# Optimization experiments

Hardware: AMD Instinct MI355X
Metric: run time of the kernel (lower is better)

## Reference

```python
import jax, jax.numpy as jnp
import numpy as np

B, N, H, HEADS, NBINS = 64, 256, 512, 8, 3
DK = H // HEADS
NEG = -1e12

def setup_inputs() -> dict:
    key = jax.random.key(0)
    ks = jax.random.split(key, 20)
    def lin(k, out_d, in_d):
        w = jax.random.normal(k, (out_d, in_d), jnp.float32) * (1.0 / np.sqrt(in_d))
        b = jnp.zeros((out_d,), jnp.float32)
        return w, b
    x = jax.random.normal(ks[0], (B, N, H), jnp.float32)
    dist = jax.random.uniform(ks[1], (B, N - 1, N - 1), jnp.float32, 0.0, 10.0)
    dist_bar = jnp.sort(jax.random.uniform(ks[2], (B, NBINS), jnp.float32, 1.0, 9.0), axis=-1)
    mask = jnp.ones((B, N, N), jnp.float32)
    Wq, bq = lin(ks[3], H, H)
    Wk, bk = lin(ks[4], H, H)
    Wv, bv = lin(ks[5], H, H)
    Wa = jnp.stack([lin(ks[6 + i], H, H)[0] for i in range(NBINS)])  # [NBINS,H,H]
    ba = jnp.zeros((NBINS, H), jnp.float32)
    Ws1, bs1 = lin(ks[10], H, NBINS * H)
    Ws2, bs2 = lin(ks[11], H, H)
    gamma = jnp.ones((H,), jnp.float32)
    beta = jnp.zeros((H,), jnp.float32)
    return dict(x=x, dist=dist, dist_bar=dist_bar, mask=mask, Wq=Wq, bq=bq, Wk=Wk, bk=bk,
                Wv=Wv, bv=bv, Wa=Wa, ba=ba, Ws1=Ws1, bs1=bs1, Ws2=Ws2, bs2=bs2,
                gamma=gamma, beta=beta)

def reference(x, dist, dist_bar, mask, Wq, bq, Wk, bk, Wv, bv, Wa, ba, Ws1, bs1, Ws2, bs2, gamma, beta):
    residual = x
    def proj(x, W, b):  # torch Linear: x @ W.T + b
        return jnp.einsum('bnd,od->bno', x, W) + b
    def heads(t):  # [B,N,H] -> [B,heads,N,dk]
        return t.reshape(B, N, HEADS, DK).transpose(0, 2, 1, 3)
    q, k, v = heads(proj(x, Wq, bq)), heads(proj(x, Wk, bk)), heads(proj(x, Wv, bv))
    scores = jnp.einsum('bhnd,bhmd->bhnm', q, k) / jnp.sqrt(jnp.float32(DK))  # [B,heads,N,N]
    # padding mask (shape [B,1,N,N] != scores shape -> masked_fill(mask==0))
    scores = jnp.where(mask[:, None] == 0, NEG, scores)
    # new_dist: super node row/col = 1, interior = dist
    new_dist = jnp.ones((B, 1, N, N), jnp.float32).at[:, :, 1:, 1:].set(dist[:, None])
    multi_out, attn_list = [], []
    for i in range(NBINS):
        cut = dist_bar[:, i][:, None, None, None]          # per-batch threshold
        dm = new_dist < cut                                 # [B,1,N,N]
        dm = dm.at[:, :, 0, :].set(True).at[:, :, :, 0].set(True)
        sd = jnp.where(dm, scores, NEG)
        attn = jax.nn.softmax(sd, axis=-1)                  # dropout: eval mode
        attn_list.append(attn)
        multi_out.append(jnp.einsum('bhnm,bhmd->bhnd', attn, v))
    x_cat = jnp.concatenate([
        jnp.einsum('bnd,od->bno', multi_out[i].transpose(0, 2, 1, 3).reshape(B, N, H), Wa[i]) + ba[i]
        for i in range(NBINS)], axis=-1)                    # [B,N,NBINS*H]
    h = jax.nn.silu(jnp.einsum('bnd,od->bno', x_cat, Ws1) + bs1)
    h = jnp.einsum('bnd,od->bno', h, Ws2) + bs2
    h = h + residual
    mu = jnp.mean(h, axis=-1, keepdims=True)
    var = jnp.var(h, axis=-1, keepdims=True)
    out = (h - mu) / jnp.sqrt(var + 1e-6) * gamma + beta
    return (out, jnp.stack(attn_list))
```

## Files before the change

kernel.cpp:

```cpp
#include <hip/hip_runtime.h>
#include <cstddef>

#define NEGV (-1e12f)


typedef __attribute__((ext_vector_type(4))) float f32x4;
typedef __attribute__((ext_vector_type(8))) __bf16 bf16x8;

__device__ __forceinline__ unsigned short f2bf(float f) {
  union { float f; unsigned u; } v; v.f = f;
  unsigned r = v.u + 0x7FFFu + ((v.u >> 16) & 1u);
  return (unsigned short)(r >> 16);
}

#define GLDS16(gp, lp)                                                      \
  __builtin_amdgcn_global_load_lds(                                         \
      (const __attribute__((address_space(1))) void*)(gp),                  \
      (__attribute__((address_space(3))) void*)(lp), 16, 0, 0)

__global__ __launch_bounds__(256) void msa_prep(
    const float* __restrict__ x, const float* __restrict__ Wq,
    const float* __restrict__ Wk, const float* __restrict__ Wv,
    const float* __restrict__ Ws2, const float* __restrict__ Ws1,
    const float* __restrict__ Wa, const float* __restrict__ bq,
    const float* __restrict__ bk, const float* __restrict__ bv,
    const float* __restrict__ ba, const float* __restrict__ bs1,
    const float* __restrict__ dist, const float* __restrict__ dist_bar,
    const float* __restrict__ maskg,
    unsigned short* __restrict__ xb, unsigned short* __restrict__ Wqkvb,
    unsigned short* __restrict__ Ws2b, unsigned short* __restrict__ Wcatb,
    float* __restrict__ bcomb, float* __restrict__ bqkv,
    unsigned long long* __restrict__ bits) {
  __shared__ float As[16][68];
  __shared__ float Bs[16][68];
  const int blk = blockIdx.x;
  const int tid = threadIdx.x;
  if (blk < 8192) {
    int i = blk * 256 + tid;
    float4 v = ((const float4*)x)[i];
    ushort4 o; o.x = f2bf(v.x); o.y = f2bf(v.y); o.z = f2bf(v.z); o.w = f2bf(v.w);
    ((ushort4*)xb)[i] = o;
    return;
  }
  if (blk < 8960) {
    int sel = (blk - 8192) >> 8;
    int i = ((blk - 8192) & 255) * 256 + tid;
    const float* src = (sel == 0) ? Wq : (sel == 1) ? Wk : Wv;
    unsigned short* dst = Wqkvb + (size_t)sel * 262144;
    float4 v = ((const float4*)src)[i];
    ushort4 o; o.x = f2bf(v.x); o.y = f2bf(v.y); o.z = f2bf(v.z); o.w = f2bf(v.w);
    ((ushort4*)dst)[i] = o;
    return;
  }
  if (blk < 9216) {
    int i = (blk - 8960) * 256 + tid;
    float4 v = ((const float4*)Ws2)[i];
    ushort4 o; o.x = f2bf(v.x); o.y = f2bf(v.y); o.z = f2bf(v.z); o.w = f2bf(v.w);
    ((ushort4*)Ws2b)[i] = o;
    return;
  }
  if (blk < 9408) {
    const int t = blk - 9216;
    const int i = t >> 6;
    const int ob = ((t >> 3) & 7) * 64, cb = (t & 7) * 64;
    const int tx = tid & 15, ty = tid >> 4;
    float acc[4][4] = {};
    for (int kt = 0; kt < 512; kt += 16) {
      __syncthreads();
      {
        int o = tid & 63, e4 = (tid >> 6) * 4;
        float4 a4 = *(const float4*)&Ws1[(size_t)(ob + o) * 1536 + i * 512 + kt + e4];
        As[e4 + 0][o] = a4.x; As[e4 + 1][o] = a4.y;
        As[e4 + 2][o] = a4.z; As[e4 + 3][o] = a4.w;
      }
      {
        int e = tid & 15, c4 = (tid >> 4) * 4;
        float4 b4 = *(const float4*)&Wa[((size_t)i << 18) + (size_t)(kt + e) * 512 + cb + c4];
        *(float4*)&Bs[e][c4] = b4;
      }
      __syncthreads();
#pragma unroll
      for (int k = 0; k < 16; ++k) {
        float a[4], bb[4];
        *(float4*)a = *(const float4*)&As[k][ty * 4];
        *(float4*)bb = *(const float4*)&Bs[k][tx * 4];
#pragma unroll
        for (int r = 0; r < 4; ++r)
#pragma unroll
          for (int c = 0; c < 4; ++c) acc[r][c] += a[r] * bb[c];
      }
    }
#pragma unroll
    for (int r = 0; r < 4; ++r)
#pragma unroll
      for (int c = 0; c < 4; ++c)
        Wcatb[(size_t)(ob + ty * 4 + r) * 1536 + i * 512 + cb + tx * 4 + c] =
            f2bf(acc[r][c]);
    return;
  }
  if (blk < 9410) {
    int o = (blk - 9408) * 256 + tid;
    float acc = bs1[o];
    for (int cidx = 0; cidx < 1536; ++cidx)
      acc += Ws1[(size_t)o * 1536 + cidx] * ba[cidx];
    bcomb[o] = acc;
    return;
  }
  if (blk < 9411) {
    for (int i = tid; i < 1536; i += 256)
      bqkv[i] = (i < 512) ? bq[i] : (i < 1024) ? bk[i - 512] : bv[i - 1024];
    return;
  }
  {
    const int gw = (blk - 9411) * 4 + (tid >> 6);
    const int lane = tid & 63;
    const int b = gw >> 8, row = gw & 255;
    const float cut0 = dist_bar[b * 3 + 0];
    const float cut1 = dist_bar[b * 3 + 1];
    const float cut2 = dist_bar[b * 3 + 2];
    const float* mrow = maskg + (size_t)b * 65536 + (size_t)row * 256;
    const int rj = (row == 0) ? 1 : row;
    const float* drow = dist + (size_t)b * 65025 + (size_t)(rj - 1) * 255;
    unsigned long long* out = bits + (size_t)gw * 12;
#pragma unroll
    for (int cc = 0; cc < 4; ++cc) {
      const int col = cc * 64 + lane;
      const int cj = (col == 0) ? 1 : col;
      float dv = drow[cj - 1];
      bool sup = (row == 0) || (col == 0);
      bool mk = (mrow[col] != 0.f);
      if (sup) dv = -1e30f;
      unsigned long long b0 = __ballot(mk && (dv < cut0));
      unsigned long long b1 = __ballot(mk && (dv < cut1));
      unsigned long long b2 = __ballot(mk && (dv < cut2));
      if (lane == 0) { out[cc] = b0; out[4 + cc] = b1; out[8 + cc] = b2; }
    }
  }
}

template <int ACT, int RES, int OBF, int BK>
__global__ __launch_bounds__(256) void msa_gemm_mfma(
    const unsigned short* __restrict__ A, int lda,
    const unsigned short* __restrict__ W, int ldw,
    const float* __restrict__ bias, const float* __restrict__ resid,
    void* __restrict__ Cout, int ldc, int Kdim) {
  constexpr int KSUB = BK / 32;
  constexpr int RPC = BK / 8;
  constexpr int CPT = (128 * RPC) / 256;
  __shared__ __align__(16) unsigned short Asm_[2][128 * BK];
  __shared__ __align__(16) unsigned short Bsm_[2][128 * BK];
  const int tid = threadIdx.x;
  const int lane = tid & 63, wv = tid >> 6;
  const int m0 = blockIdx.x * 128, n0 = blockIdx.y * 128;
  const int wr = wv >> 1, wc = wv & 1;
  const int fr = lane & 15, fq = lane >> 4;
  f32x4 acc[4][4] = {};
  const unsigned short* Ag[CPT];
  const unsigned short* Wg[CPT];
#pragma unroll
  for (int i = 0; i < CPT; ++i) {
    int c = tid + i * 256;
    int row = c / RPC, j = c % RPC;
    Ag[i] = A + (size_t)(m0 + row) * lda + j * 8;
    Wg[i] = W + (size_t)(n0 + row) * ldw + j * 8;
  }
#pragma unroll
  for (int i = 0; i < CPT; ++i) {
    GLDS16(Ag[i], &Asm_[0][(tid + i * 256) * 8]);
    GLDS16(Wg[i], &Bsm_[0][(tid + i * 256) * 8]);
  }
  __syncthreads();
  int cur = 0;
  for (int kt = 0; kt < Kdim; kt += BK) {
    if (kt + BK < Kdim) {
      const int nx = cur ^ 1, k2 = kt + BK;
#pragma unroll
      for (int i = 0; i < CPT; ++i) {
        GLDS16(Ag[i] + k2, &Asm_[nx][(tid + i * 256) * 8]);
        GLDS16(Wg[i] + k2, &Bsm_[nx][(tid + i * 256) * 8]);
      }
    }
#pragma unroll
    for (int ks = 0; ks < KSUB; ++ks) {
      bf16x8 af[4], bfr[4];
#pragma unroll
      for (int mf = 0; mf < 4; ++mf)
        af[mf] = *(const bf16x8*)&Asm_[cur][(wr * 64 + mf * 16 + fr) * BK + ks * 32 + fq * 8];
#pragma unroll
      for (int nf = 0; nf < 4; ++nf)
        bfr[nf] = *(const bf16x8*)&Bsm_[cur][(wc * 64 + nf * 16 + fr) * BK + ks * 32 + fq * 8];
#pragma unroll
      for (int mf = 0; mf < 4; ++mf)
#pragma unroll
        for (int nf = 0; nf < 4; ++nf)
          acc[mf][nf] = __builtin_amdgcn_mfma_f32_16x16x32_bf16(
              af[mf], bfr[nf], acc[mf][nf], 0, 0, 0);
    }
    __syncthreads();
    cur ^= 1;
  }
#pragma unroll
  for (int mf = 0; mf < 4; ++mf) {
#pragma unroll
    for (int nf = 0; nf < 4; ++nf) {
      const int n = n0 + wc * 64 + nf * 16 + fr;
      const float bval = bias[n];
#pragma unroll
      for (int r = 0; r < 4; ++r) {
        const int m = m0 + wr * 64 + mf * 16 + fq * 4 + r;
        float val = acc[mf][nf][r] + bval;
        if (ACT == 1) val = val / (1.f + __expf(-val));
        if (RES == 1) val += resid[(size_t)m * ldc + n];
        if (OBF == 1)
          ((unsigned short*)Cout)[(size_t)m * ldc + n] = f2bf(val);
        else
          ((float*)Cout)[(size_t)m * ldc + n] = val;
      }
    }
  }
}

__global__ __launch_bounds__(512) void msa_fused(
    const unsigned short* __restrict__ qkvb,
    const unsigned long long* __restrict__ bits,
    float* __restrict__ attn_out, unsigned short* __restrict__ mob) {
  const int blk = blockIdx.x;
  const int b = (blk & 7) * 8 + (blk >> 6);
  const int h = (blk >> 3) & 7;
  __shared__ __align__(16) unsigned short Kl[256][72];
  __shared__ __align__(16) unsigned short Vt[64][264];
  __shared__ __align__(16) unsigned short Pl[8][16][264];
  const int tid = threadIdx.x;
  const int wv = tid >> 6, lane = tid & 63;
  const int l15 = lane & 15, fq = lane >> 4;
  {
    const unsigned short* kgp = qkvb + (size_t)(b * 256) * 1536 + 512 + h * 64;
#pragma unroll
    for (int i = 0; i < 4; ++i) {
      int s = tid + i * 512;
      int row = s >> 3, c8 = (s & 7) << 3;
      *(uint4*)&Kl[row][c8] = *(const uint4*)&kgp[(size_t)row * 1536 + c8];
    }
  }
  {
    int rv = tid & 255, half = tid >> 8;
    const unsigned short* vgp =
        qkvb + (size_t)(b * 256 + rv) * 1536 + 1024 + h * 64 + half * 32;
#pragma unroll
    for (int j4 = 0; j4 < 4; ++j4) {
      unsigned short tmp[8];
      *(uint4*)tmp = *(const uint4*)&vgp[j4 * 8];
#pragma unroll
      for (int j = 0; j < 8; ++j) Vt[half * 32 + j4 * 8 + j][rv] = tmp[j];
    }
  }
  __syncthreads();
#pragma unroll
  for (int mf = 0; mf < 2; ++mf) {
    const int r0 = wv * 32 + mf * 16;
    const unsigned short* qgp =
        qkvb + (size_t)(b * 256 + r0 + l15) * 1536 + h * 64 + fq * 8;
    bf16x8 aq0 = *(const bf16x8*)qgp;
    bf16x8 aq1 = *(const bf16x8*)(qgp + 32);
    f32x4 accs[16];
#pragma unroll
    for (int nt = 0; nt < 16; ++nt) {
      bf16x8 bk0 = *(const bf16x8*)&Kl[nt * 16 + l15][fq * 8];
      bf16x8 bk1 = *(const bf16x8*)&Kl[nt * 16 + l15][32 + fq * 8];
      f32x4 a = {};
      a = __builtin_amdgcn_mfma_f32_16x16x32_bf16(aq0, bk0, a, 0, 0, 0);
      a = __builtin_amdgcn_mfma_f32_16x16x32_bf16(aq1, bk1, a, 0, 0, 0);
      accs[nt] = a;
    }
#pragma unroll
    for (int bin = 0; bin < 3; ++bin) {
      float* pbase = attn_out + ((size_t)((bin * 64 + b) * 8 + h)) * 65536;
#pragma unroll
      for (int r = 0; r < 4; ++r) {
        const int row = r0 + fq * 4 + r;
        const unsigned long long* bw =
            bits + (size_t)(b * 256 + row) * 12 + bin * 4;
        const unsigned long long w0 = bw[0], w1 = bw[1], w2 = bw[2], w3 = bw[3];
        float p[16];
        float m = -3e38f;
#pragma unroll
        for (int nt = 0; nt < 16; ++nt) {
          unsigned long long w = (nt < 4) ? w0 : (nt < 8) ? w1 : (nt < 12) ? w2 : w3;
          unsigned keep = (unsigned)(w >> ((nt & 3) * 16 + l15)) & 1u;
          float sv = accs[nt][r] * 0.125f;
          p[nt] = keep ? sv : NEGV;
          m = fmaxf(m, p[nt]);
        }
        m = fmaxf(m, __shfl_xor(m, 1));
        m = fmaxf(m, __shfl_xor(m, 2));
        m = fmaxf(m, __shfl_xor(m, 4));
        m = fmaxf(m, __shfl_xor(m, 8));
        float sum = 0.f;
#pragma unroll
        for (int nt = 0; nt < 16; ++nt) { p[nt] = __expf(p[nt] - m); sum += p[nt]; }
        sum += __shfl_xor(sum, 1);
        sum += __shfl_xor(sum, 2);
        sum += __shfl_xor(sum, 4);
        sum += __shfl_xor(sum, 8);
        const float inv = 1.f / sum;
        float* prow = pbase + (size_t)row * 256 + l15;
#pragma unroll
        for (int nt = 0; nt < 16; ++nt) {
          float val = p[nt] * inv;
          prow[nt * 16] = val;
          Pl[wv][fq * 4 + r][nt * 16 + l15] = f2bf(val);
        }
      }
      asm volatile("s_waitcnt lgkmcnt(0)" ::: "memory");
      f32x4 acco[4] = {};
#pragma unroll
      for (int c = 0; c < 8; ++c) {
        bf16x8 pa = *(const bf16x8*)&Pl[wv][l15][c * 32 + fq * 8];
#pragma unroll
        for (int nf = 0; nf < 4; ++nf) {
          bf16x8 bv = *(const bf16x8*)&Vt[nf * 16 + l15][c * 32 + fq * 8];
          acco[nf] = __builtin_amdgcn_mfma_f32_16x16x32_bf16(pa, bv, acco[nf], 0, 0, 0);
        }
      }
#pragma unroll
      for (int nf = 0; nf < 4; ++nf)
#pragma unroll
        for (int r = 0; r < 4; ++r)
          mob[((size_t)(b * 256 + r0 + fq * 4 + r) * 3 + bin) * 512 +
              h * 64 + nf * 16 + l15] = f2bf(acco[nf][r]);
    }
  }
}

__global__ __launch_bounds__(256) void msa_mlp2ln(
    const unsigned short* __restrict__ h1b, const unsigned short* __restrict__ Ws2b,
    const float* __restrict__ bs2, const float* __restrict__ x,
    const float* __restrict__ gamma, const float* __restrict__ beta,
    float* __restrict__ outp) {
  __shared__ __align__(16) unsigned short Al[32 * 32];
  __shared__ __align__(16) unsigned short Bl[512 * 32];
  __shared__ float red[2][2][32];
  const int tid = threadIdx.x;
  const int lane = tid & 63, wv = tid >> 6;
  const int wr = wv >> 1, wc = wv & 1;
  const int l15 = lane & 15, fq = lane >> 4;
  const int m0 = blockIdx.x * 32;
  f32x4 acc[16] = {};
  for (int kt = 0; kt < 512; kt += 32) {
    if (tid < 128) {
      int row = tid >> 2, c8 = (tid & 3) * 8;
      GLDS16(h1b + (size_t)(m0 + row) * 512 + kt + c8, &Al[tid * 8]);
    }
#pragma unroll
    for (int i = 0; i < 8; ++i) {
      int c = tid + i * 256;
      int row = c >> 2, c8 = (c & 3) * 8;
      GLDS16(Ws2b + (size_t)row * 512 + kt + c8, &Bl[c * 8]);
    }
    __syncthreads();
    bf16x8 af = *(const bf16x8*)&Al[(wr * 16 + l15) * 32 + fq * 8];
#pragma unroll
    for (int nt = 0; nt < 16; ++nt) {
      bf16x8 bfr = *(const bf16x8*)&Bl[(wc * 256 + nt * 16 + l15) * 32 + fq * 8];
      acc[nt] = __builtin_amdgcn_mfma_f32_16x16x32_bf16(af, bfr, acc[nt], 0, 0, 0);
    }
    __syncthreads();
  }
  float vals[16][4];
#pragma unroll
  for (int nt = 0; nt < 16; ++nt) {
    const int n = wc * 256 + nt * 16 + l15;
    const float bval = bs2[n];
#pragma unroll
    for (int r = 0; r < 4; ++r) {
      const int m = m0 + wr * 16 + fq * 4 + r;
      vals[nt][r] = acc[nt][r] + bval + x[(size_t)m * 512 + n];
    }
  }
  const int ridx = wr * 16 + fq * 4;
#pragma unroll
  for (int r = 0; r < 4; ++r) {
    float s = 0.f;
#pragma unroll
    for (int nt = 0; nt < 16; ++nt) s += vals[nt][r];
    s += __shfl_xor(s, 1); s += __shfl_xor(s, 2);
    s += __shfl_xor(s, 4); s += __shfl_xor(s, 8);
    if (l15 == 0) red[0][wc][ridx + r] = s;
  }
  __syncthreads();
  float mu[4];
#pragma unroll
  for (int r = 0; r < 4; ++r)
    mu[r] = (red[0][0][ridx + r] + red[0][1][ridx + r]) * (1.f / 512.f);
#pragma unroll
  for (int r = 0; r < 4; ++r) {
    float s = 0.f;
#pragma unroll
    for (int nt = 0; nt < 16; ++nt) {
      float d = vals[nt][r] - mu[r];
      s += d * d;
    }
    s += __shfl_xor(s, 1); s += __shfl_xor(s, 2);
    s += __shfl_xor(s, 4); s += __shfl_xor(s, 8);
    if (l15 == 0) red[1][wc][ridx + r] = s;
  }
  __syncthreads();
  float iv[4];
#pragma unroll
  for (int r = 0; r < 4; ++r) {
    float var = (red[1][0][ridx + r] + red[1][1][ridx + r]) * (1.f / 512.f);
    iv[r] = 1.f / sqrtf(var + 1e-6f);
  }
#pragma unroll
  for (int nt = 0; nt < 16; ++nt) {
    const int n = wc * 256 + nt * 16 + l15;
    const float g = gamma[n], be = beta[n];
#pragma unroll
    for (int r = 0; r < 4; ++r) {
      const int m = m0 + wr * 16 + fq * 4 + r;
      outp[(size_t)m * 512 + n] = (vals[nt][r] - mu[r]) * iv[r] * g + be;
    }
  }
}

extern "C" void kernel_launch(void* const* d_in, const int* in_sizes, int n_in,
                              void* d_out, int out_size, void* d_ws, size_t ws_size,
                              hipStream_t stream) {
  (void)in_sizes; (void)n_in; (void)out_size; (void)ws_size;
  const float* x        = (const float*)d_in[0];
  const float* dist     = (const float*)d_in[1];
  const float* dist_bar = (const float*)d_in[2];
  const float* mask     = (const float*)d_in[3];
  const float* Wq  = (const float*)d_in[4];  const float* bq  = (const float*)d_in[5];
  const float* Wk  = (const float*)d_in[6];  const float* bk  = (const float*)d_in[7];
  const float* Wv  = (const float*)d_in[8];  const float* bv  = (const float*)d_in[9];
  const float* Wa  = (const float*)d_in[10]; const float* ba  = (const float*)d_in[11];
  const float* Ws1 = (const float*)d_in[12]; const float* bs1 = (const float*)d_in[13];
  const float* Ws2 = (const float*)d_in[14]; const float* bs2 = (const float*)d_in[15];
  const float* gamma = (const float*)d_in[16]; const float* beta = (const float*)d_in[17];

  char* w8 = (char*)d_ws;
  const size_t SZ = 8388608;
  unsigned short* qkvb = (unsigned short*)(w8 + 0);
  unsigned short* mob  = (unsigned short*)(w8 + 50331648);
  unsigned short* xb   = (unsigned short*)(w8 + 100663296);
  unsigned short* Wqkvb= (unsigned short*)(w8 + 117440512);
  unsigned short* Ws2b = (unsigned short*)(w8 + 119013376);
  unsigned short* Wcatb= (unsigned short*)(w8 + 119537664);
  float* bcomb = (float*)(w8 + 121110528);
  float* bqkv  = (float*)(w8 + 121112576);
  unsigned long long* bits = (unsigned long long*)(w8 + 121118720);
  unsigned short* h1b = qkvb;
  float* outp = (float*)d_out;
  float* attn = outp + SZ;

  msa_prep<<<13507, 256, 0, stream>>>(x, Wq, Wk, Wv, Ws2, Ws1, Wa, bq, bk, bv,
                                      ba, bs1, dist, dist_bar, mask,
                                      xb, Wqkvb, Ws2b, Wcatb, bcomb, bqkv, bits);

  msa_gemm_mfma<0, 0, 1, 32><<<dim3(128, 12), 256, 0, stream>>>(
      xb, 512, Wqkvb, 512, bqkv, nullptr, qkvb, 1536, 512);

  msa_fused<<<512, 512, 0, stream>>>(qkvb, bits, attn, mob);

  msa_gemm_mfma<1, 0, 1, 64><<<dim3(128, 4), 256, 0, stream>>>(
      mob, 1536, Wcatb, 1536, bcomb, nullptr, h1b, 512, 1536);

  msa_mlp2ln<<<512, 256, 0, stream>>>(h1b, Ws2b, bs2, x, gamma, beta, outp);
}
```

Before: 323.0 us.

## Transpose QK^T MFMA so each lane owns a query row, vectorize prob stores

Swaps the MFMA operands for the score product so each lane holds four consecutive key columns of one query row. Softmax then reduces across only two cross-lane shuffles per bin instead of four per row, and the attention probabilities are written to global memory as float4 vectors. The bf16 probabilities go to a compact, XOR-swizzled LDS tile to avoid bank conflicts, and extra waitcnt/sched barriers are added to keep LDS reuse across bins correct. The cost is higher register pressure from holding 64 probability values per lane.

```diff
diff --git a/kernel.cpp b/kernel.cpp
--- a/kernel.cpp
+++ b/kernel.cpp
@@ -229,7 +229,7 @@
   const int h = (blk >> 3) & 7;
   __shared__ __align__(16) unsigned short Kl[256][72];
   __shared__ __align__(16) unsigned short Vt[64][264];
-  __shared__ __align__(16) unsigned short Pl[8][16][264];
+  __shared__ __align__(16) unsigned short Pl[8][16][256];
   const int tid = threadIdx.x;
   const int wv = tid >> 6, lane = tid & 63;
   const int l15 = lane & 15, fq = lane >> 4;
@@ -255,11 +255,14 @@
     }
   }
   __syncthreads();
+  char* plbase = (char*)&Pl[wv][0][0];
+  const int swz = ((l15 & 1) << 6) | ((l15 & 2) << 4);
 #pragma unroll
   for (int mf = 0; mf < 2; ++mf) {
     const int r0 = wv * 32 + mf * 16;
+    const int q = r0 + l15;
     const unsigned short* qgp =
-        qkvb + (size_t)(b * 256 + r0 + l15) * 1536 + h * 64 + fq * 8;
+        qkvb + (size_t)(b * 256 + q) * 1536 + h * 64 + fq * 8;
     bf16x8 aq0 = *(const bf16x8*)qgp;
     bf16x8 aq1 = *(const bf16x8*)(qgp + 32);
     f32x4 accs[16];
@@ -268,54 +271,63 @@
       bf16x8 bk0 = *(const bf16x8*)&Kl[nt * 16 + l15][fq * 8];
       bf16x8 bk1 = *(const bf16x8*)&Kl[nt * 16 + l15][32 + fq * 8];
       f32x4 a = {};
-      a = __builtin_amdgcn_mfma_f32_16x16x32_bf16(aq0, bk0, a, 0, 0, 0);
-      a = __builtin_amdgcn_mfma_f32_16x16x32_bf16(aq1, bk1, a, 0, 0, 0);
+      a = __builtin_amdgcn_mfma_f32_16x16x32_bf16(bk0, aq0, a, 0, 0, 0);
+      a = __builtin_amdgcn_mfma_f32_16x16x32_bf16(bk1, aq1, a, 0, 0, 0);
       accs[nt] = a;
     }
+    const unsigned long long* brow = bits + (size_t)(b * 256 + q) * 12;
 #pragma unroll
     for (int bin = 0; bin < 3; ++bin) {
-      float* pbase = attn_out + ((size_t)((bin * 64 + b) * 8 + h)) * 65536;
-#pragma unroll
-      for (int r = 0; r < 4; ++r) {
-        const int row = r0 + fq * 4 + r;
-        const unsigned long long* bw =
-            bits + (size_t)(b * 256 + row) * 12 + bin * 4;
-        const unsigned long long w0 = bw[0], w1 = bw[1], w2 = bw[2], w3 = bw[3];
-        float p[16];
-        float m = -3e38f;
-#pragma unroll
-        for (int nt = 0; nt < 16; ++nt) {
-          unsigned long long w = (nt < 4) ? w0 : (nt < 8) ? w1 : (nt < 12) ? w2 : w3;
-          unsigned keep = (unsigned)(w >> ((nt & 3) * 16 + l15)) & 1u;
+      const unsigned long long w0 = brow[bin * 4 + 0];
+      const unsigned long long w1 = brow[bin * 4 + 1];
+      const unsigned long long w2 = brow[bin * 4 + 2];
+      const unsigned long long w3 = brow[bin * 4 + 3];
+      f32x4 p[16];
+      float m = -3e38f;
+#pragma unroll
+      for (int nt = 0; nt < 16; ++nt) {
+        unsigned long long w = (nt < 4) ? w0 : (nt < 8) ? w1 : (nt < 12) ? w2 : w3;
+#pragma unroll
+        for (int r = 0; r < 4; ++r) {
+          unsigned keep = (unsigned)(w >> (16 * (nt & 3) + 4 * fq + r)) & 1u;
           float sv = accs[nt][r] * 0.125f;
-          p[nt] = keep ? sv : NEGV;
-          m = fmaxf(m, p[nt]);
+          float v = keep ? sv : NEGV;
+          p[nt][r] = v;
+          m = fmaxf(m, v);
         }
-        m = fmaxf(m, __shfl_xor(m, 1));
-        m = fmaxf(m, __shfl_xor(m, 2));
-        m = fmaxf(m, __shfl_xor(m, 4));
-        m = fmaxf(m, __shfl_xor(m, 8));
-        float sum = 0.f;
-#pragma unroll
-        for (int nt = 0; nt < 16; ++nt) { p[nt] = __expf(p[nt] - m); sum += p[nt]; }
-        sum += __shfl_xor(sum, 1);
-        sum += __shfl_xor(sum, 2);
-        sum += __shfl_xor(sum, 4);
-        sum += __shfl_xor(sum, 8);
-        const float inv = 1.f / sum;
-        float* prow = pbase + (size_t)row * 256 + l15;
-#pragma unroll
-        for (int nt = 0; nt < 16; ++nt) {
-          float val = p[nt] * inv;
-          prow[nt * 16] = val;
-          Pl[wv][fq * 4 + r][nt * 16 + l15] = f2bf(val);
+      }
+      m = fmaxf(m, __shfl_xor(m, 16));
+      m = fmaxf(m, __shfl_xor(m, 32));
+      float sum = 0.f;
+#pragma unroll
+      for (int nt = 0; nt < 16; ++nt)
+#pragma unroll
+        for (int r = 0; r < 4; ++r) {
+          p[nt][r] = __expf(p[nt][r] - m);
+          sum += p[nt][r];
         }
+      sum += __shfl_xor(sum, 16);
+      sum += __shfl_xor(sum, 32);
+      const float inv = 1.f / sum;
+      float* prow = attn_out + ((size_t)((bin * 64 + b) * 8 + h)) * 65536 +
+                    (size_t)q * 256;
+#pragma unroll
+      for (int nt = 0; nt < 16; ++nt) {
+        float v0 = p[nt][0] * inv, v1 = p[nt][1] * inv;
+        float v2 = p[nt][2] * inv, v3 = p[nt][3] * inv;
+        *(float4*)(prow + nt * 16 + fq * 4) = make_float4(v0, v1, v2, v3);
+        unsigned short u[4];
+        u[0] = f2bf(v0); u[1] = f2bf(v1); u[2] = f2bf(v2); u[3] = f2bf(v3);
+        int wb = (l15 << 9) | (nt << 5) | (fq << 3);
+        *(uint2*)(plbase + (wb ^ swz)) = *(const uint2*)u;
       }
       asm volatile("s_waitcnt lgkmcnt(0)" ::: "memory");
+      __builtin_amdgcn_sched_barrier(0);
       f32x4 acco[4] = {};
 #pragma unroll
       for (int c = 0; c < 8; ++c) {
-        bf16x8 pa = *(const bf16x8*)&Pl[wv][l15][c * 32 + fq * 8];
+        int rb = (l15 << 9) | (c << 6) | (fq << 4);
+        bf16x8 pa = *(const bf16x8*)(plbase + (rb ^ swz));
 #pragma unroll
         for (int nf = 0; nf < 4; ++nf) {
           bf16x8 bv = *(const bf16x8*)&Vt[nf * 16 + l15][c * 32 + fq * 8];
@@ -328,6 +340,8 @@
         for (int r = 0; r < 4; ++r)
           mob[((size_t)(b * 256 + r0 + fq * 4 + r) * 3 + bin) * 512 +
               h * 64 + nf * 16 + l15] = f2bf(acco[nf][r]);
+      asm volatile("s_waitcnt lgkmcnt(0)" ::: "memory");
+      __builtin_amdgcn_sched_barrier(0);
     }
   }
 }
```

Result: no change. 325.3 us (+0.7%).
